# Kernel tuning notes

Hardware: AMD Instinct MI355X
Metric: run time of the kernel (lower is better)

## Reference

```python
import jax, jax.numpy as jnp
import numpy as np

K = 5  # up_kernel

def bilinear(x, hw):
    # torch F.interpolate bilinear, align_corners=False (half-pixel), no antialias
    return jax.image.resize(x, x.shape[:2] + hw, method='linear', antialias=False)

def nearest2x(x):
    return jnp.repeat(jnp.repeat(x, 2, axis=2), 2, axis=3)

def conv3x3(x, w, b):
    y = jax.lax.conv_general_dilated(x, w, (1, 1), [(1, 1), (1, 1)],
                                     dimension_numbers=('NCHW', 'OIHW', 'NCHW'))
    return y + b[None, :, None, None]

def carafe(x, mask):
    # x: [N,C,H,W]; mask: [N,K*K,H,W] softmax-normalized. scale_factor=1, up_group=1.
    N, C, H, W = x.shape
    r = K // 2
    xp = jnp.pad(x, ((0, 0), (0, 0), (r, r), (r, r)))
    out = jnp.zeros_like(x)
    idx = 0
    for di in range(K):
        for dj in range(K):
            out = out + xp[:, :, di:di + H, dj:dj + W] * mask[:, idx:idx + 1]
            idx += 1
    return out

def setup_inputs() -> dict:
    key = jax.random.key(0)
    ks = jax.random.split(key, 6)
    feat = jax.random.normal(ks[0], (1, 32, 96, 96), jnp.float32)
    seg = jax.random.normal(ks[1], (1, 19, 96, 96), jnp.float32)
    img = jax.random.uniform(ks[2], (1, 3, 384, 384), jnp.float32)
    w_enc0 = jax.random.normal(ks[3], (25, 35, 3, 3), jnp.float32) * 0.05
    b_enc0 = jnp.zeros((25,), jnp.float32)
    w_enc1 = jax.random.normal(ks[4], (25, 35, 3, 3), jnp.float32) * 0.05
    b_enc1 = jnp.zeros((25,), jnp.float32)
    return {'feat': feat, 'seg': seg, 'img': img,
            'w_enc0': w_enc0, 'b_enc0': b_enc0, 'w_enc1': w_enc1, 'b_enc1': b_enc1}

def reference(feat, seg, img, w_enc0, b_enc0, w_enc1, b_enc1):
    weights = [(w_enc0, b_enc0), (w_enc1, b_enc1)]
    for i in range(2):
        Hf, Wf = feat.shape[-2], feat.shape[-1]
        resized_img = bilinear(img, (2 * Hf, 2 * Wf))
        # high-boost filtering: img_hf = img - lowpass(img) + img
        lr = bilinear(resized_img, (Hf, Wf))
        lr = bilinear(lr, (2 * Hf, 2 * Wf))
        img_hf = 2.0 * resized_img - lr
        feat_up = nearest2x(feat)
        seg_up = nearest2x(seg)
        w, b = weights[i]
        mask = conv3x3(jnp.concatenate([feat_up, img_hf], axis=1), w, b)
        # kernel_normalizer: pixel_shuffle(1)=identity, softmax over the 25 kernel taps
        mask = jax.nn.softmax(mask, axis=1)
        seg = carafe(seg_up, mask)
        feat = carafe(feat_up, mask)
    return seg
```

## Files before the change

kernel.cpp:

```cpp
#include <hip/hip_runtime.h>


__global__ __launch_bounds__(256) void repack_kernel(
    const float* __restrict__ w0s, const float* __restrict__ w1s,
    float* __restrict__ W2a, float* __restrict__ wTha,
    float* __restrict__ W2b, float* __restrict__ wThb) {
  int i = blockIdx.x * 256 + threadIdx.x;
  const float* w; float* W2; float* wTh; int k = i;
  if (i < 13475) { w = w0s; W2 = W2a; wTh = wTha; }
  else { k = i - 13475; if (k >= 13475) return; w = w1s; W2 = W2b; wTh = wThb; }
  if (k < 12800) {
    int oc = k % 25; int j = k / 25;
    int src = j & 3; j >>= 2;
    int ic = j & 31; int p = j >> 5;
    int py = p >> 1, px = p & 1;
    int a = src >> 1, b = src & 1;
    float s = 0.f;
    for (int ky = 0; ky < 3; ++ky) {
      int rs = (py == 0) ? (ky >= 1) : (ky >= 2);
      if (rs != a) continue;
      for (int kx = 0; kx < 3; ++kx) {
        int cs = (px == 0) ? (kx >= 1) : (kx >= 2);
        if (cs != b) continue;
        s += w[oc * 315 + ic * 9 + ky * 3 + kx];
      }
    }
    W2[k] = s;
  } else {
    int kk = k - 12800;
    int oc = kk % 25; int j = kk / 25;
    int h = j % 3; int tap = j / 3;
    wTh[kk] = w[oc * 315 + (32 + h) * 9 + tap];
  }
}

__global__ __launch_bounds__(256) void down2_kernel(
    const float* __restrict__ in, float* __restrict__ out) {
  int idx = blockIdx.x * 256 + threadIdx.x;
  if (idx >= 3 * 192 * 192) return;
  int x = idx % 192; int t = idx / 192; int y = t % 192; int c = t / 192;
  const float* p = in + (c * 384 + 2 * y) * 384 + 2 * x;
  out[idx] = 0.25f * (p[0] + p[1] + p[384] + p[385]);
}

__global__ __launch_bounds__(256) void hf0_kernel(
    const float* __restrict__ I192, float* __restrict__ out) {
  int idx = blockIdx.x * 256 + threadIdx.x;
  if (idx >= 3 * 192 * 192) return;
  int x = idx % 192; int t = idx / 192; int y = t % 192; int c = t / 192;
  int m = y >> 1; int ya, yb; float wya, wyb;
  if ((y & 1) == 0) { ya = m - 1 < 0 ? 0 : m - 1; yb = m; wya = 0.25f; wyb = 0.75f; }
  else             { ya = m; yb = m + 1 > 95 ? 95 : m + 1; wya = 0.75f; wyb = 0.25f; }
  int n = x >> 1; int xa, xb; float wxa, wxb;
  if ((x & 1) == 0) { xa = n - 1 < 0 ? 0 : n - 1; xb = n; wxa = 0.25f; wxb = 0.75f; }
  else             { xa = n; xb = n + 1 > 95 ? 95 : n + 1; wxa = 0.75f; wxb = 0.25f; }
  const float* base = I192 + c * 192 * 192;
  auto I96v = [&](int mm, int nn) {
    const float* p = base + (2 * mm) * 192 + 2 * nn;
    return 0.25f * (p[0] + p[1] + p[192] + p[193]);
  };
  float up = wya * (wxa * I96v(ya, xa) + wxb * I96v(ya, xb))
           + wyb * (wxa * I96v(yb, xa) + wxb * I96v(yb, xb));
  out[idx] = 2.0f * base[y * 192 + x] - up;
}

__global__ __launch_bounds__(256) void highboost_kernel(
    const float* __restrict__ base, const float* __restrict__ lr,
    float* __restrict__ out) {
  const int H = 192, OW = 384;
  int idx = blockIdx.x * 256 + threadIdx.x;
  if (idx >= 3 * 384 * 384) return;
  int x = idx % OW; int t = idx / OW; int y = t % 384; int c = t / 384;
  int m = y >> 1; int ya, yb; float wya, wyb;
  if ((y & 1) == 0) { ya = m - 1 < 0 ? 0 : m - 1; yb = m; wya = 0.25f; wyb = 0.75f; }
  else             { ya = m; yb = m + 1 >= H ? H - 1 : m + 1; wya = 0.75f; wyb = 0.25f; }
  int n = x >> 1; int xa, xb; float wxa, wxb;
  if ((x & 1) == 0) { xa = n - 1 < 0 ? 0 : n - 1; xb = n; wxa = 0.25f; wxb = 0.75f; }
  else             { xa = n; xb = n + 1 >= H ? H - 1 : n + 1; wxa = 0.75f; wxb = 0.25f; }
  const float* p = lr + c * H * H;
  float up = wya * (wxa * p[ya * H + xa] + wxb * p[ya * H + xb])
           + wyb * (wxa * p[yb * H + xa] + wxb * p[yb * H + xb]);
  out[idx] = 2.0f * base[idx] - up;
}

__global__ __launch_bounds__(512, 4) void conv_softmax_kernel(
    const float* __restrict__ feat, const float* __restrict__ hf,
    const float* __restrict__ W2, const float* __restrict__ wTh,
    const float* __restrict__ b, float* __restrict__ CW,
    int Hf, int Wf) {
  const int OH = 2 * Hf, OW = 2 * Wf, Np = OH * OW, fplane = Hf * Wf;
  __shared__ float red[8][64][26];

  const int t = threadIdx.x;
  const int lane = t & 63;
  const int s = __builtin_amdgcn_readfirstlane(t >> 6);
  const int par = blockIdx.x & 3;
  const int bt = blockIdx.x >> 2;
  const int TW = Wf >> 5;
  const int gx0 = (bt % TW) << 5;
  const int gy0 = (bt / TW) << 1;
  const int py = par >> 1, px = par & 1;
  const int gy = gy0 + (lane >> 5);
  const int gx = gx0 + (lane & 31);

  int r0 = gy - 1 + py; const bool zr0 = (r0 < 0);      if (zr0) r0 = 0;
  int r1 = gy + py;     const bool zr1 = (r1 >= Hf);    if (zr1) r1 = Hf - 1;
  int c0 = gx - 1 + px; const bool zc0 = (c0 < 0);      if (zc0) c0 = 0;
  int c1 = gx + px;     const bool zc1 = (c1 >= Wf);    if (zc1) c1 = Wf - 1;
  const int o00 = r0 * Wf + c0, o01 = r0 * Wf + c1;
  const int o10 = r1 * Wf + c0, o11 = r1 * Wf + c1;

  float acc[25];
#pragma unroll
  for (int oc = 0; oc < 25; ++oc) acc[oc] = 0.f;

  const int fbeg = s == 0 ? 0 : s == 1 ? 2 : s == 2 ? 4 : s == 3 ? 6
                 : s == 4 ? 12 : s == 5 ? 17 : s == 6 ? 22 : 27;
  const int fend = s == 0 ? 2 : s == 1 ? 4 : s == 2 ? 6 : s == 3 ? 12
                 : s == 4 ? 17 : s == 5 ? 22 : s == 6 ? 27 : 32;

  for (int ic = fbeg; ic < fend; ++ic) {
    const float* fp = feat + ic * fplane;
    float v00 = (zr0 | zc0) ? 0.f : fp[o00];
    float v01 = (zr0 | zc1) ? 0.f : fp[o01];
    float v10 = (zr1 | zc0) ? 0.f : fp[o10];
    float v11 = (zr1 | zc1) ? 0.f : fp[o11];
    const float* wp = W2 + (size_t)((par * 32 + ic) * 4) * 25;
#pragma unroll
    for (int oc = 0; oc < 25; ++oc)
      acc[oc] += v00 * wp[oc] + v01 * wp[25 + oc] + v10 * wp[50 + oc] + v11 * wp[75 + oc];
  }

  if (s < 3) {
    const int x = 2 * gx + px, y = 2 * gy + py;
    const float* hp = hf + s * Np;
#pragma unroll
    for (int ky = 0; ky < 3; ++ky) {
      int yy = y + ky - 1;
      bool vy = (yy >= 0) && (yy < OH);
      int yo = (vy ? yy : 0) * OW;
#pragma unroll
      for (int kx = 0; kx < 3; ++kx) {
        int xx = x + kx - 1;
        bool vv = vy && (xx >= 0) && (xx < OW);
        float v = vv ? hp[yo + (vv ? xx : 0)] : 0.f;
        const float* wp = wTh + ((ky * 3 + kx) * 3 + s) * 25;
#pragma unroll
        for (int oc = 0; oc < 25; ++oc) acc[oc] = fmaf(v, wp[oc], acc[oc]);
      }
    }
  }

#pragma unroll
  for (int oc = 0; oc < 25; ++oc) red[s][lane][oc] = acc[oc];
  __syncthreads();
  for (int i = t; i < 1600; i += 512) {
    int oc = i % 25, p2 = i / 25;
    float sum = red[0][p2][oc];
#pragma unroll
    for (int k = 1; k < 8; ++k) sum += red[k][p2][oc];
    red[0][p2][oc] = sum + b[oc];
  }
  __syncthreads();

  if (t < 64) {
    const int gy2 = gy0 + (t >> 5), gx2 = gx0 + (t & 31);
    const int y = 2 * gy2 + py, x = 2 * gx2 + px;
    float m[25];
#pragma unroll
    for (int oc = 0; oc < 25; ++oc) m[oc] = red[0][t][oc];
    float mx = m[0];
#pragma unroll
    for (int oc = 1; oc < 25; ++oc) mx = fmaxf(mx, m[oc]);
    float ssum = 0.f;
#pragma unroll
    for (int oc = 0; oc < 25; ++oc) { m[oc] = __expf(m[oc] - mx); ssum += m[oc]; }
    float inv = 1.0f / ssum;

    bool vy[5], vx[5];
#pragma unroll
    for (int d = 0; d < 5; ++d) {
      vy[d] = (unsigned)(y + d - 2) < (unsigned)OH;
      vx[d] = (unsigned)(x + d - 2) < (unsigned)OW;
    }
    float rs[3][5];
    if (py == 0) {
#pragma unroll
      for (int dj = 0; dj < 5; ++dj) {
        float m0 = (vy[0] && vx[dj]) ? m[0 + dj] : 0.f;
        float m1 = (vy[1] && vx[dj]) ? m[5 + dj] : 0.f;
        float m2 = (vy[2] && vx[dj]) ? m[10 + dj] : 0.f;
        float m3 = (vy[3] && vx[dj]) ? m[15 + dj] : 0.f;
        float m4 = (vy[4] && vx[dj]) ? m[20 + dj] : 0.f;
        rs[0][dj] = m0 + m1; rs[1][dj] = m2 + m3; rs[2][dj] = m4;
      }
    } else {
#pragma unroll
      for (int dj = 0; dj < 5; ++dj) {
        float m0 = (vy[0] && vx[dj]) ? m[0 + dj] : 0.f;
        float m1 = (vy[1] && vx[dj]) ? m[5 + dj] : 0.f;
        float m2 = (vy[2] && vx[dj]) ? m[10 + dj] : 0.f;
        float m3 = (vy[3] && vx[dj]) ? m[15 + dj] : 0.f;
        float m4 = (vy[4] && vx[dj]) ? m[20 + dj] : 0.f;
        rs[0][dj] = m0; rs[1][dj] = m1 + m2; rs[2][dj] = m3 + m4;
      }
    }
    float cw[9];
#pragma unroll
    for (int r = 0; r < 3; ++r) {
      if (px == 0) {
        cw[r * 3 + 0] = rs[r][0] + rs[r][1];
        cw[r * 3 + 1] = rs[r][2] + rs[r][3];
        cw[r * 3 + 2] = rs[r][4];
      } else {
        cw[r * 3 + 0] = rs[r][0];
        cw[r * 3 + 1] = rs[r][1] + rs[r][2];
        cw[r * 3 + 2] = rs[r][3] + rs[r][4];
      }
    }
    const int pix = y * OW + x;
#pragma unroll
    for (int tap = 0; tap < 9; ++tap) CW[tap * Np + pix] = cw[tap] * inv;
  }
}

__global__ __launch_bounds__(256) void carafe_kernel(
    const float* __restrict__ CW,
    const float* __restrict__ in0, float* __restrict__ out0, int C0,
    const float* __restrict__ in1, float* __restrict__ out1, int C1,
    int CS, int Hf, int Wf) {
  const int OW = 2 * Wf;
  const int Np = 4 * Hf * Wf;
  int pix = blockIdx.x * 256 + threadIdx.x;
  if (pix >= Np) return;
  int x = pix % OW, y = pix / OW;
  int ry0 = (y >> 1) - 1, rx0 = (x >> 1) - 1;
  int sy[3], sx[3];
#pragma unroll
  for (int i = 0; i < 3; ++i) {
    int v = ry0 + i; sy[i] = v < 0 ? 0 : (v >= Hf ? Hf - 1 : v);
    int u = rx0 + i; sx[i] = u < 0 ? 0 : (u >= Wf ? Wf - 1 : u);
  }
  float cw[9];
#pragma unroll
  for (int i = 0; i < 9; ++i) cw[i] = CW[i * Np + pix];
  const int fplane = Hf * Wf;
  int cbeg = blockIdx.y * CS;
  int cend = cbeg + CS; int Ct = C0 + C1; if (cend > Ct) cend = Ct;
  for (int c = cbeg; c < cend; ++c) {
    const float* p; float* q;
    if (c < C0) { p = in0 + c * fplane; q = out0 + c * Np; }
    else        { p = in1 + (c - C0) * fplane; q = out1 + (c - C0) * Np; }
    const float* r0 = p + sy[0] * Wf;
    const float* r1 = p + sy[1] * Wf;
    const float* r2 = p + sy[2] * Wf;
    float acc = cw[0] * r0[sx[0]] + cw[1] * r0[sx[1]] + cw[2] * r0[sx[2]]
              + cw[3] * r1[sx[0]] + cw[4] * r1[sx[1]] + cw[5] * r1[sx[2]]
              + cw[6] * r2[sx[0]] + cw[7] * r2[sx[1]] + cw[8] * r2[sx[2]];
    q[pix] = acc;
  }
}

extern "C" void kernel_launch(void* const* d_in, const int* in_sizes, int n_in,
                              void* d_out, int out_size, void* d_ws, size_t ws_size,
                              hipStream_t stream) {
  (void)in_sizes; (void)n_in; (void)out_size; (void)ws_size;
  const float* feat = (const float*)d_in[0];
  const float* seg  = (const float*)d_in[1];
  const float* img  = (const float*)d_in[2];
  const float* w0   = (const float*)d_in[3];
  const float* b0   = (const float*)d_in[4];
  const float* w1   = (const float*)d_in[5];
  const float* b1   = (const float*)d_in[6];
  float* out = (float*)d_out;

  float* ws   = (float*)d_ws;
  float* I192 = ws;
  float* HF   = I192 + 3 * 192 * 192;
  float* CWb  = HF   + 3 * 384 * 384;
  float* F1   = CWb  + 9 * 384 * 384;
  float* S1   = F1   + 32 * 192 * 192;
  float* W2_0 = S1   + 19 * 192 * 192;
  float* WTH0 = W2_0 + 12800;
  float* W2_1 = WTH0 + 675;
  float* WTH1 = W2_1 + 12800;

  repack_kernel<<<106, 256, 0, stream>>>(w0, w1, W2_0, WTH0, W2_1, WTH1);
  down2_kernel<<<432, 256, 0, stream>>>(img, I192);

  hf0_kernel<<<432, 256, 0, stream>>>(I192, HF);
  conv_softmax_kernel<<<4 * 48 * 3, 512, 0, stream>>>(
      feat, HF, W2_0, WTH0, b0, CWb, 96, 96);
  carafe_kernel<<<dim3(144, 3), 256, 0, stream>>>(
      CWb, seg, S1, 19, feat, F1, 32, 17, 96, 96);

  highboost_kernel<<<1728, 256, 0, stream>>>(img, I192, HF);
  conv_softmax_kernel<<<4 * 96 * 6, 512, 0, stream>>>(
      F1, HF, W2_1, WTH1, b1, CWb, 192, 192);
  carafe_kernel<<<dim3(576, 2), 256, 0, stream>>>(
      CWb, S1, out, 19, nullptr, nullptr, 0, 10, 192, 192);
}
```

Measured before the change: 175.6 us.

## Stage conv input tiles in LDS and give each wave one parity

The conv+softmax kernel now loads a haloed 32-channel feature tile and a 3-channel high-pass tile into shared memory once per block. Each of the four waves handles one output parity over all input channels, which removes the cross-wave LDS reduction and the second barrier. Softmax and the tap folding run in every thread instead of only the first 64, and block indices are swizzled across the grid. The trade-off is four times fewer blocks, with each thread doing the full channel loop serially, which means less parallelism on small grids.

Result: slower. 184.9 us (+5.3%).

```diff
diff --git a/kernel.cpp b/kernel.cpp
--- a/kernel.cpp
+++ b/kernel.cpp
@@ -83,145 +83,127 @@
   out[idx] = 2.0f * base[idx] - up;
 }
 
-__global__ __launch_bounds__(512, 4) void conv_softmax_kernel(
+__global__ __launch_bounds__(256, 4) void conv_softmax_kernel(
     const float* __restrict__ feat, const float* __restrict__ hf,
     const float* __restrict__ W2, const float* __restrict__ wTh,
     const float* __restrict__ b, float* __restrict__ CW,
     int Hf, int Wf) {
-  const int OH = 2 * Hf, OW = 2 * Wf, Np = OH * OW, fplane = Hf * Wf;
-  __shared__ float red[8][64][26];
-
+  const int OH = 2 * Hf, OW = 2 * Wf, Np = OH * OW, fp = Hf * Wf;
+  __shared__ float sf[32 * 144];
+  __shared__ float sh[3 * 408];
   const int t = threadIdx.x;
+  const int TW = Wf >> 5;
+  const int wg = ((blockIdx.x & 7) * (gridDim.x >> 3)) + (blockIdx.x >> 3);
+  const int tx = wg % TW, ty = wg / TW;
+  const int gx0 = tx << 5, gy0 = ty << 1;
+
+  for (int i = t; i < 32 * 136; i += 256) {
+    int ic = i / 136, rem = i - ic * 136;
+    int r = rem / 34, c = rem - r * 34;
+    int gr = gy0 - 1 + r, gc = gx0 - 1 + c;
+    float v = 0.f;
+    if ((unsigned)gr < (unsigned)Hf && (unsigned)gc < (unsigned)Wf)
+      v = feat[ic * fp + gr * Wf + gc];
+    sf[ic * 144 + r * 36 + c] = v;
+  }
+  for (int i = t; i < 3 * 396; i += 256) {
+    int ch = i / 396, rem = i - ch * 396;
+    int R = rem / 66, C = rem - R * 66;
+    int gr = 2 * gy0 - 1 + R, gc = 2 * gx0 - 1 + C;
+    float v = 0.f;
+    if ((unsigned)gr < (unsigned)OH && (unsigned)gc < (unsigned)OW)
+      v = hf[ch * Np + gr * OW + gc];
+    sh[ch * 408 + R * 68 + C] = v;
+  }
+  __syncthreads();
+
+  const int w = __builtin_amdgcn_readfirstlane(t >> 6);
   const int lane = t & 63;
-  const int s = __builtin_amdgcn_readfirstlane(t >> 6);
-  const int par = blockIdx.x & 3;
-  const int bt = blockIdx.x >> 2;
-  const int TW = Wf >> 5;
-  const int gx0 = (bt % TW) << 5;
-  const int gy0 = (bt / TW) << 1;
-  const int py = par >> 1, px = par & 1;
-  const int gy = gy0 + (lane >> 5);
-  const int gx = gx0 + (lane & 31);
-
-  int r0 = gy - 1 + py; const bool zr0 = (r0 < 0);      if (zr0) r0 = 0;
-  int r1 = gy + py;     const bool zr1 = (r1 >= Hf);    if (zr1) r1 = Hf - 1;
-  int c0 = gx - 1 + px; const bool zc0 = (c0 < 0);      if (zc0) c0 = 0;
-  int c1 = gx + px;     const bool zc1 = (c1 >= Wf);    if (zc1) c1 = Wf - 1;
-  const int o00 = r0 * Wf + c0, o01 = r0 * Wf + c1;
-  const int o10 = r1 * Wf + c0, o11 = r1 * Wf + c1;
+  const int py = w >> 1, px = w & 1;
+  const int ly = lane >> 5, lx = lane & 31;
+  const int lr0 = ly + py;
+  const int lc0 = lx + px;
 
   float acc[25];
 #pragma unroll
-  for (int oc = 0; oc < 25; ++oc) acc[oc] = 0.f;
-
-  const int fbeg = s == 0 ? 0 : s == 1 ? 2 : s == 2 ? 4 : s == 3 ? 6
-                 : s == 4 ? 12 : s == 5 ? 17 : s == 6 ? 22 : 27;
-  const int fend = s == 0 ? 2 : s == 1 ? 4 : s == 2 ? 6 : s == 3 ? 12
-                 : s == 4 ? 17 : s == 5 ? 22 : s == 6 ? 27 : 32;
-
-  for (int ic = fbeg; ic < fend; ++ic) {
-    const float* fp = feat + ic * fplane;
-    float v00 = (zr0 | zc0) ? 0.f : fp[o00];
-    float v01 = (zr0 | zc1) ? 0.f : fp[o01];
-    float v10 = (zr1 | zc0) ? 0.f : fp[o10];
-    float v11 = (zr1 | zc1) ? 0.f : fp[o11];
-    const float* wp = W2 + (size_t)((par * 32 + ic) * 4) * 25;
+  for (int oc = 0; oc < 25; ++oc) acc[oc] = b[oc];
+
+  for (int ic = 0; ic < 32; ++ic) {
+    const float* base = sf + ic * 144 + lr0 * 36 + lc0;
+    float v00 = base[0], v01 = base[1], v10 = base[36], v11 = base[37];
+    const float* wp = W2 + (size_t)((w * 32 + ic) * 4) * 25;
 #pragma unroll
     for (int oc = 0; oc < 25; ++oc)
       acc[oc] += v00 * wp[oc] + v01 * wp[25 + oc] + v10 * wp[50 + oc] + v11 * wp[75 + oc];
   }
-
-  if (s < 3) {
-    const int x = 2 * gx + px, y = 2 * gy + py;
-    const float* hp = hf + s * Np;
-#pragma unroll
-    for (int ky = 0; ky < 3; ++ky) {
-      int yy = y + ky - 1;
-      bool vy = (yy >= 0) && (yy < OH);
-      int yo = (vy ? yy : 0) * OW;
-#pragma unroll
-      for (int kx = 0; kx < 3; ++kx) {
-        int xx = x + kx - 1;
-        bool vv = vy && (xx >= 0) && (xx < OW);
-        float v = vv ? hp[yo + (vv ? xx : 0)] : 0.f;
-        const float* wp = wTh + ((ky * 3 + kx) * 3 + s) * 25;
-#pragma unroll
-        for (int oc = 0; oc < 25; ++oc) acc[oc] = fmaf(v, wp[oc], acc[oc]);
-      }
-    }
-  }
-
-#pragma unroll
-  for (int oc = 0; oc < 25; ++oc) red[s][lane][oc] = acc[oc];
-  __syncthreads();
-  for (int i = t; i < 1600; i += 512) {
-    int oc = i % 25, p2 = i / 25;
-    float sum = red[0][p2][oc];
-#pragma unroll
-    for (int k = 1; k < 8; ++k) sum += red[k][p2][oc];
-    red[0][p2][oc] = sum + b[oc];
-  }
-  __syncthreads();
-
-  if (t < 64) {
-    const int gy2 = gy0 + (t >> 5), gx2 = gx0 + (t & 31);
-    const int y = 2 * gy2 + py, x = 2 * gx2 + px;
-    float m[25];
-#pragma unroll
-    for (int oc = 0; oc < 25; ++oc) m[oc] = red[0][t][oc];
-    float mx = m[0];
-#pragma unroll
-    for (int oc = 1; oc < 25; ++oc) mx = fmaxf(mx, m[oc]);
-    float ssum = 0.f;
-#pragma unroll
-    for (int oc = 0; oc < 25; ++oc) { m[oc] = __expf(m[oc] - mx); ssum += m[oc]; }
-    float inv = 1.0f / ssum;
-
-    bool vy[5], vx[5];
-#pragma unroll
-    for (int d = 0; d < 5; ++d) {
-      vy[d] = (unsigned)(y + d - 2) < (unsigned)OH;
-      vx[d] = (unsigned)(x + d - 2) < (unsigned)OW;
-    }
-    float rs[3][5];
-    if (py == 0) {
-#pragma unroll
-      for (int dj = 0; dj < 5; ++dj) {
-        float m0 = (vy[0] && vx[dj]) ? m[0 + dj] : 0.f;
-        float m1 = (vy[1] && vx[dj]) ? m[5 + dj] : 0.f;
-        float m2 = (vy[2] && vx[dj]) ? m[10 + dj] : 0.f;
-        float m3 = (vy[3] && vx[dj]) ? m[15 + dj] : 0.f;
-        float m4 = (vy[4] && vx[dj]) ? m[20 + dj] : 0.f;
-        rs[0][dj] = m0 + m1; rs[1][dj] = m2 + m3; rs[2][dj] = m4;
-      }
+  {
+    const int R0 = 2 * ly + py, C0 = 2 * lx + px;
+#pragma unroll
+    for (int ky = 0; ky < 3; ++ky)
+#pragma unroll
+      for (int kx = 0; kx < 3; ++kx)
+#pragma unroll
+        for (int ch = 0; ch < 3; ++ch) {
+          float v = sh[ch * 408 + (R0 + ky) * 68 + (C0 + kx)];
+          const float* wp = wTh + ((ky * 3 + kx) * 3 + ch) * 25;
+#pragma unroll
+          for (int oc = 0; oc < 25; ++oc) acc[oc] = fmaf(v, wp[oc], acc[oc]);
+        }
+  }
+
+  const int y = 2 * (gy0 + ly) + py, x = 2 * (gx0 + lx) + px;
+  float mx = acc[0];
+#pragma unroll
+  for (int oc = 1; oc < 25; ++oc) mx = fmaxf(mx, acc[oc]);
+  float ssum = 0.f;
+#pragma unroll
+  for (int oc = 0; oc < 25; ++oc) { acc[oc] = __expf(acc[oc] - mx); ssum += acc[oc]; }
+  float inv = 1.0f / ssum;
+
+  bool vy[5], vx[5];
+#pragma unroll
+  for (int d = 0; d < 5; ++d) {
+    vy[d] = (unsigned)(y + d - 2) < (unsigned)OH;
+    vx[d] = (unsigned)(x + d - 2) < (unsigned)OW;
+  }
+  float rs[3][5];
+  if (py == 0) {
+#pragma unroll
+    for (int dj = 0; dj < 5; ++dj) {
+      float m0 = (vy[0] && vx[dj]) ? acc[0 + dj] : 0.f;
+      float m1 = (vy[1] && vx[dj]) ? acc[5 + dj] : 0.f;
+      float m2 = (vy[2] && vx[dj]) ? acc[10 + dj] : 0.f;
+      float m3 = (vy[3] && vx[dj]) ? acc[15 + dj] : 0.f;
+      float m4 = (vy[4] && vx[dj]) ? acc[20 + dj] : 0.f;
+      rs[0][dj] = m0 + m1; rs[1][dj] = m2 + m3; rs[2][dj] = m4;
+    }
+  } else {
+#pragma unroll
+    for (int dj = 0; dj < 5; ++dj) {
+      float m0 = (vy[0] && vx[dj]) ? acc[0 + dj] : 0.f;
+      float m1 = (vy[1] && vx[dj]) ? acc[5 + dj] : 0.f;
+      float m2 = (vy[2] && vx[dj]) ? acc[10 + dj] : 0.f;
+      float m3 = (vy[3] && vx[dj]) ? acc[15 + dj] : 0.f;
+      float m4 = (vy[4] && vx[dj]) ? acc[20 + dj] : 0.f;
+      rs[0][dj] = m0; rs[1][dj] = m1 + m2; rs[2][dj] = m3 + m4;
+    }
+  }
+  float cw[9];
+#pragma unroll
+  for (int r = 0; r < 3; ++r) {
+    if (px == 0) {
+      cw[r * 3 + 0] = rs[r][0] + rs[r][1];
+      cw[r * 3 + 1] = rs[r][2] + rs[r][3];
+      cw[r * 3 + 2] = rs[r][4];
     } else {
-#pragma unroll
-      for (int dj = 0; dj < 5; ++dj) {
-        float m0 = (vy[0] && vx[dj]) ? m[0 + dj] : 0.f;
-        float m1 = (vy[1] && vx[dj]) ? m[5 + dj] : 0.f;
-        float m2 = (vy[2] && vx[dj]) ? m[10 + dj] : 0.f;
-        float m3 = (vy[3] && vx[dj]) ? m[15 + dj] : 0.f;
-        float m4 = (vy[4] && vx[dj]) ? m[20 + dj] : 0.f;
-        rs[0][dj] = m0; rs[1][dj] = m1 + m2; rs[2][dj] = m3 + m4;
-      }
-    }
-    float cw[9];
-#pragma unroll
-    for (int r = 0; r < 3; ++r) {
-      if (px == 0) {
-        cw[r * 3 + 0] = rs[r][0] + rs[r][1];
-        cw[r * 3 + 1] = rs[r][2] + rs[r][3];
-        cw[r * 3 + 2] = rs[r][4];
-      } else {
-        cw[r * 3 + 0] = rs[r][0];
-        cw[r * 3 + 1] = rs[r][1] + rs[r][2];
-        cw[r * 3 + 2] = rs[r][3] + rs[r][4];
-      }
-    }
-    const int pix = y * OW + x;
-#pragma unroll
-    for (int tap = 0; tap < 9; ++tap) CW[tap * Np + pix] = cw[tap] * inv;
-  }
+      cw[r * 3 + 0] = rs[r][0];
+      cw[r * 3 + 1] = rs[r][1] + rs[r][2];
+      cw[r * 3 + 2] = rs[r][3] + rs[r][4];
+    }
+  }
+  const int pix = y * OW + x;
+#pragma unroll
+  for (int tap = 0; tap < 9; ++tap) CW[tap * Np + pix] = cw[tap] * inv;
 }
 
 __global__ __launch_bounds__(256) void carafe_kernel(
@@ -289,13 +271,13 @@
   down2_kernel<<<432, 256, 0, stream>>>(img, I192);
 
   hf0_kernel<<<432, 256, 0, stream>>>(I192, HF);
-  conv_softmax_kernel<<<4 * 48 * 3, 512, 0, stream>>>(
+  conv_softmax_kernel<<<48 * 3, 256, 0, stream>>>(
       feat, HF, W2_0, WTH0, b0, CWb, 96, 96);
   carafe_kernel<<<dim3(144, 3), 256, 0, stream>>>(
       CWb, seg, S1, 19, feat, F1, 32, 17, 96, 96);
 
   highboost_kernel<<<1728, 256, 0, stream>>>(img, I192, HF);
-  conv_softmax_kernel<<<4 * 96 * 6, 512, 0, stream>>>(
+  conv_softmax_kernel<<<96 * 6, 256, 0, stream>>>(
       F1, HF, W2_1, WTH1, b1, CWb, 192, 192);
   carafe_kernel<<<dim3(576, 2), 256, 0, stream>>>(
       CWb, S1, out, 19, nullptr, nullptr, 0, 10, 192, 192);
```
